# Performance work log

Measured on AMD Instinct MI355X. Metric: run time of the kernel, lower is better.

## Reference

```python
import jax, jax.numpy as jnp
import numpy as np

B, T, D, H = 512, 256, 64, 128


def _uniform(key, shape, stdv):
    return jax.random.uniform(key, shape, jnp.float32, -stdv, stdv)


def setup_inputs() -> dict:
    key = jax.random.key(0)
    ks = jax.random.split(key, 20)
    x_t = jax.random.normal(ks[0], (B, T, D), jnp.float32)
    masks = (jax.random.uniform(ks[1], (B, T, D)) < 0.8).astype(jnp.float32)
    deltas = jax.random.uniform(ks[2], (B, T, D), jnp.float32)
    sH = 1.0 / np.sqrt(H)
    sD = 1.0 / np.sqrt(D)
    return {
        "x_t": x_t, "masks": masks, "deltas": deltas,
        # TemporalDecay h: [H, D]
        "Wdh": _uniform(ks[3], (H, D), sH), "bdh": _uniform(ks[4], (H,), sH),
        # TemporalDecay x (diag): [D, D]
        "Wdx": _uniform(ks[5], (D, D), sD), "bdx": _uniform(ks[6], (D,), sD),
        # hist_reg Linear(H -> D)
        "Whr": _uniform(ks[7], (D, H), sH), "bhr": _uniform(ks[8], (D,), sH),
        "Wfr": _uniform(ks[9], (D, D), sD), "bfr": _uniform(ks[10], (D,), sD),
        # weight_combine Linear(2D -> D)
        "Wwc": _uniform(ks[11], (D, 2 * D), 1.0 / np.sqrt(2 * D)),
        "bwc": _uniform(ks[12], (D,), 1.0 / np.sqrt(2 * D)),
        # LSTMCell(2D -> H)
        "W_ih": _uniform(ks[13], (4 * H, 2 * D), sH), "W_hh": _uniform(ks[14], (4 * H, H), sH),
        "b_ih": _uniform(ks[15], (4 * H,), sH), "b_hh": _uniform(ks[16], (4 * H,), sH),
    }


def reference(x_t, masks, deltas, Wdh, bdh, Wdx, bdx, Whr, bhr, Wfr, bfr, Wwc, bwc, W_ih, W_hh, b_ih, b_hh):
    Bv, Tv, Dv = x_t.shape
    Hv = Wdh.shape[0]
    eye = jnp.eye(Dv, dtype=x_t.dtype)
    Wdx_m = Wdx * eye              # diagonal temporal decay
    Wfr_m = Wfr * (1.0 - eye)

    def step(carry, xs):
        h, c, loss = carry
        x, m, d = xs
        gamma_h = jnp.exp(-jax.nn.relu(d @ Wdh.T + bdh))   # [B,H]
        gamma_x = jnp.exp(-jax.nn.relu(d @ Wdx_m.T + bdx))  # [B,D]
        h = h * gamma_h
        x_h = h @ Whr.T + bhr
        msum = jnp.sum(m) + 1e-5
        loss = loss + jnp.sum(jnp.abs(x - x_h) * m) / msum
        x_c = m * x + (1.0 - m) * x_h
        z_h = x_c @ Wfr_m.T + bfr
        loss = loss + jnp.sum(jnp.abs(x - z_h) * m) / msum
        alpha = jnp.concatenate([gamma_x, m], axis=1) @ Wwc.T + bwc
        c_h = alpha * z_h + (1.0 - alpha) * x_h
        loss = loss + jnp.sum(jnp.abs(x - c_h) * m) / msum
        c_c = m * x + (1.0 - m) * c_h
        inp = jnp.concatenate([c_c, m], axis=1)            # [B,2D]
        gates = inp @ W_ih.T + b_ih + h @ W_hh.T + b_hh    # [B,4H]
        i, f, g, o = jnp.split(gates, 4, axis=1)
        c = jax.nn.sigmoid(f) * c + jax.nn.sigmoid(i) * jnp.tanh(g)
        h = jax.nn.sigmoid(o) * jnp.tanh(c)
        return (h, c, loss), c_c

    h0 = jnp.zeros((Bv, Hv), x_t.dtype)
    c0 = jnp.zeros((Bv, Hv), x_t.dtype)
    xs = (jnp.swapaxes(x_t, 0, 1), jnp.swapaxes(masks, 0, 1), jnp.swapaxes(deltas, 0, 1))
    (h, c, loss), imps = jax.lax.scan(step, (h0, c0, jnp.float32(0.0)), xs)
    imputations = jnp.swapaxes(imps, 0, 1)                 # [B,T,D]
    return loss / Tv, imputations
```

## Files before the change

### kernel.cpp

```cpp
#include <hip/hip_runtime.h>
#include <hip/hip_bf16.h>

typedef __bf16 bf16x8 __attribute__((ext_vector_type(8)));
typedef float f32x4 __attribute__((ext_vector_type(4)));

#define NB 512
#define NT 256
#define ND 64
#define NH 128
#define PART_IDX 256
#define FLAG_IDX 320

__device__ __forceinline__ float bf2f(__hip_bfloat16 v){ return __bfloat162float(v); }
__device__ __forceinline__ __hip_bfloat16 f2bf(float v){ return __float2bfloat16(v); }

__device__ __forceinline__ float ldF(const float* p){ return *p; }
__device__ __forceinline__ float ldF(const __hip_bfloat16* p){ return __bfloat162float(*p); }
__device__ __forceinline__ void  stF(float* p, float v){ *p = v; }
__device__ __forceinline__ void  stF(__hip_bfloat16* p, float v){ *p = __float2bfloat16(v); }

__device__ __forceinline__ bf16x8 ldfrag(const __hip_bfloat16* p){
    return *reinterpret_cast<const bf16x8*>(p);
}
__device__ __forceinline__ bf16x8 ldfrag(const float* p){
    f32x4 a = *reinterpret_cast<const f32x4*>(p);
    f32x4 b = *reinterpret_cast<const f32x4*>(p + 4);
    bf16x8 r;
    #pragma unroll
    for (int i = 0; i < 4; ++i){
        __hip_bfloat16 ha = __float2bfloat16(a[i]);
        __hip_bfloat16 hb = __float2bfloat16(b[i]);
        r[i]   = *reinterpret_cast<__bf16*>(&ha);
        r[4+i] = *reinterpret_cast<__bf16*>(&hb);
    }
    return r;
}
__device__ __forceinline__ bf16x8 ldbf8(const __hip_bfloat16* p){
    return *reinterpret_cast<const bf16x8*>(p);
}

template<typename T> __device__ __forceinline__ float wantFlag(){ return sizeof(T)==4 ? 1.f : 0.f; }

__device__ __forceinline__ f32x4 mfma16(bf16x8 a, bf16x8 b, f32x4 c){
    return __builtin_amdgcn_mfma_f32_16x16x32_bf16(a, b, c, 0, 0, 0);
}
__device__ __forceinline__ float fsig(float x){ return 1.f/(1.f+__expf(-x)); }
__device__ __forceinline__ float ftanh(float x){ return 1.f - 2.f/(__expf(2.f*x)+1.f); }

__global__ void detect_kernel(const void* __restrict__ x, float* __restrict__ WS){
    if (threadIdx.x == 0 && blockIdx.x == 0){
        const unsigned short* u = (const unsigned short*)x;
        int weird = 0;
        for (int i = 0; i < 256; ++i){
            unsigned e = (u[i] >> 7) & 0xFF;
            if (e == 0xFF || e >= 0x8A || (e != 0 && e <= 0x5A)) ++weird;
        }
        WS[FLAG_IDX] = (weird >= 16) ? 1.f : 0.f;
    }
}

template<typename T>
__global__ __launch_bounds__(256) void msum_kernel(const T* __restrict__ M,
                                                   float* __restrict__ WS){
    if (WS[FLAG_IDX] != wantFlag<T>()) return;
    int t = blockIdx.x;
    int tid = threadIdx.x;
    int col = tid & 63;
    int bg  = tid >> 6;
    float s = 0.f;
    for (int b = bg; b < NB; b += 4)
        s += ldF(&M[((size_t)b*NT + t)*ND + col]);
    #pragma unroll
    for (int off = 32; off > 0; off >>= 1) s += __shfl_down(s, off);
    __shared__ float r4[4];
    if ((tid & 63) == 0) r4[bg] = s;
    __syncthreads();
    if (tid == 0) WS[t] = 1.f / (r4[0] + r4[1] + r4[2] + r4[3] + 1e-5f);
}

template<typename T>
__device__ __forceinline__ f32x4 gates_tile(const T* __restrict__ wih_row,
                                            const T* __restrict__ whh_row,
                                            int lg, const bf16x8 af[8]){
    f32x4 acc = {0.f,0.f,0.f,0.f};
    acc = mfma16(af[0], ldfrag(wih_row + 0  + lg*8), acc);
    acc = mfma16(af[1], ldfrag(wih_row + 32 + lg*8), acc);
    acc = mfma16(af[2], ldfrag(wih_row + 64 + lg*8), acc);
    acc = mfma16(af[3], ldfrag(wih_row + 96 + lg*8), acc);
    acc = mfma16(af[4], ldfrag(whh_row + 0  + lg*8), acc);
    acc = mfma16(af[5], ldfrag(whh_row + 32 + lg*8), acc);
    acc = mfma16(af[6], ldfrag(whh_row + 64 + lg*8), acc);
    acc = mfma16(af[7], ldfrag(whh_row + 96 + lg*8), acc);
    return acc;
}

template<typename T>
__global__ __launch_bounds__(512, 2) void brits_main(
    const T* __restrict__ X,  const T* __restrict__ M,
    const T* __restrict__ DL,
    const T* __restrict__ Wdh, const T* __restrict__ bdh,
    const T* __restrict__ Wdx, const T* __restrict__ bdx,
    const T* __restrict__ Whr, const T* __restrict__ bhr,
    const T* __restrict__ Wfr, const T* __restrict__ bfr,
    const T* __restrict__ Wwc, const T* __restrict__ bwc,
    const T* __restrict__ Wih, const T* __restrict__ Whh,
    const T* __restrict__ bih, const T* __restrict__ bhh,
    T* __restrict__ OUT, float* __restrict__ WS)
{
    if (WS[FLAG_IDX] != wantFlag<T>()) return;

    __shared__ __align__(16) __hip_bfloat16 sAg[16][264];
    __shared__ __align__(16) __hip_bfloat16 sAal[16][136];
    __shared__ __align__(16) __hip_bfloat16 sXc[16][72];
    __shared__ __align__(16) T sX[16][72];
    __shared__ float sXh[16][68];
    __shared__ float sZh[16][68];
    __shared__ float sAl[16][68];
    __shared__ float sWdg[64];
    __shared__ float sBdx[64];
    __shared__ float sRed[8];

    const int tid = threadIdx.x;
    const int w  = tid >> 6;
    const int l  = tid & 63;
    const int lr = l & 15;
    const int lg = l >> 4;
    const int b0 = blockIdx.x * 16;

    if (tid < 64){ sWdg[tid] = ldF(&Wdx[tid*ND + tid]); sBdx[tid] = ldF(&bdx[tid]); }

    const int hcol = 16*w + lr;
    const float bdh_r = ldF(&bdh[hcol]);
    const float gb_i = ldF(&bih[hcol])      + ldF(&bhh[hcol]);
    const float gb_f = ldF(&bih[NH+hcol])   + ldF(&bhh[NH+hcol]);
    const float gb_g = ldF(&bih[2*NH+hcol]) + ldF(&bhh[2*NH+hcol]);
    const float gb_o = ldF(&bih[3*NH+hcol]) + ldF(&bhh[3*NH+hcol]);

    bf16x8 pB0 = ldfrag(Wdh + (size_t)hcol*ND + lg*8);
    bf16x8 pB1 = ldfrag(Wdh + (size_t)hcol*ND + 32 + lg*8);
    bf16x8 qB0 = {}, qB1 = {}, qB2 = {}, qB3 = {}, rB0 = {}, rB1 = {};
    float b1_r = 0.f, b2_r = 0.f, b3_r = 0.f;
    int dcol;
    if (w < 4){
        dcol = 16*w + lr;
        b1_r = ldF(&bhr[dcol]);  b2_r = ldF(&bfr[dcol]);
        qB0 = ldfrag(Whr + (size_t)dcol*NH + lg*8);
        qB1 = ldfrag(Whr + (size_t)dcol*NH + 32 + lg*8);
        qB2 = ldfrag(Whr + (size_t)dcol*NH + 64 + lg*8);
        qB3 = ldfrag(Whr + (size_t)dcol*NH + 96 + lg*8);
        rB0 = ldfrag(Wfr + (size_t)dcol*ND + lg*8);
        rB1 = ldfrag(Wfr + (size_t)dcol*ND + 32 + lg*8);
        int kb0 = lg*8;      if (dcol >= kb0 && dcol < kb0+8) rB0[dcol-kb0] = (__bf16)0.f;
        int kb1 = 32 + lg*8; if (dcol >= kb1 && dcol < kb1+8) rB1[dcol-kb1] = (__bf16)0.f;
    } else {
        dcol = 16*(w-4) + lr;
        b3_r = ldF(&bwc[dcol]);
        qB0 = ldfrag(Wwc + (size_t)dcol*2*ND + lg*8);
        qB1 = ldfrag(Wwc + (size_t)dcol*2*ND + 32 + lg*8);
        qB2 = ldfrag(Wwc + (size_t)dcol*2*ND + 64 + lg*8);
        qB3 = ldfrag(Wwc + (size_t)dcol*2*ND + 96 + lg*8);
    }

    float hreg[4] = {0.f,0.f,0.f,0.f};
    float creg[4] = {0.f,0.f,0.f,0.f};
    float lacc = 0.f;

    const int r0 = tid >> 5;
    const int c0 = (tid & 31) * 2;

    __syncthreads();

    #pragma unroll 1
    for (int t = 0; t < NT; ++t){
        const float inv_ms = WS[t];
        {
            const T* drow = DL + ((size_t)(b0+lr)*NT + t)*ND;
            f32x4 acc = {0.f,0.f,0.f,0.f};
            acc = mfma16(ldfrag(drow + lg*8), pB0, acc);
            acc = mfma16(ldfrag(drow + 32 + lg*8), pB1, acc);
            #pragma unroll
            for (int r = 0; r < 4; ++r){
                float gm = __expf(-fmaxf(acc[r] + bdh_r, 0.f));
                hreg[r] *= gm;
                sAg[lg*4+r][128 + hcol] = f2bf(hreg[r]);
            }
            #pragma unroll
            for (int e = 0; e < 2; ++e){
                int row = r0, col = c0 + e;
                size_t g = ((size_t)(b0+row)*NT + t)*ND + col;
                float dv = ldF(&DL[g]);
                float gx = __expf(-fmaxf(dv*sWdg[col] + sBdx[col], 0.f));
                sAal[row][col] = f2bf(gx);
                float mv = ldF(&M[g]);
                sAal[row][64+col] = f2bf(mv);
                sAg[row][64+col]  = f2bf(mv);
                sX[row][col]      = X[g];
            }
        }
        __syncthreads();
        if (w < 4){
            f32x4 acc = {0.f,0.f,0.f,0.f};
            acc = mfma16(ldbf8(&sAg[lr][128 + 0  + lg*8]), qB0, acc);
            acc = mfma16(ldbf8(&sAg[lr][128 + 32 + lg*8]), qB1, acc);
            acc = mfma16(ldbf8(&sAg[lr][128 + 64 + lg*8]), qB2, acc);
            acc = mfma16(ldbf8(&sAg[lr][128 + 96 + lg*8]), qB3, acc);
            #pragma unroll
            for (int r = 0; r < 4; ++r){
                int row = lg*4 + r;
                float xh = acc[r] + b1_r;
                sXh[row][dcol] = xh;
                float mv = bf2f(sAg[row][64+dcol]);
                float xv = ldF(&sX[row][dcol]);
                float xc = mv*xv + (1.f-mv)*xh;
                sXc[row][dcol] = f2bf(xc);
                lacc += fabsf(xv - xh) * mv * inv_ms;
            }
        } else {
            f32x4 acc = {0.f,0.f,0.f,0.f};
            acc = mfma16(ldbf8(&sAal[lr][0  + lg*8]), qB0, acc);
            acc = mfma16(ldbf8(&sAal[lr][32 + lg*8]), qB1, acc);
            acc = mfma16(ldbf8(&sAal[lr][64 + lg*8]), qB2, acc);
            acc = mfma16(ldbf8(&sAal[lr][96 + lg*8]), qB3, acc);
            #pragma unroll
            for (int r = 0; r < 4; ++r) sAl[lg*4+r][dcol] = acc[r] + b3_r;
        }
        __syncthreads();
        if (w < 4){
            f32x4 acc = {0.f,0.f,0.f,0.f};
            acc = mfma16(ldbf8(&sXc[lr][0  + lg*8]), rB0, acc);
            acc = mfma16(ldbf8(&sXc[lr][32 + lg*8]), rB1, acc);
            #pragma unroll
            for (int r = 0; r < 4; ++r) sZh[lg*4+r][dcol] = acc[r] + b2_r;
        }
        __syncthreads();
        {
            #pragma unroll
            for (int e = 0; e < 2; ++e){
                int row = r0, col = c0 + e;
                size_t g = ((size_t)(b0+row)*NT + t)*ND + col;
                float xv = ldF(&sX[row][col]);
                float mv = bf2f(sAg[row][64+col]);
                float zh = sZh[row][col];
                float xh = sXh[row][col];
                float al = sAl[row][col];
                float ch = al*zh + (1.f-al)*xh;
                lacc += (fabsf(xv - zh) + fabsf(xv - ch)) * mv * inv_ms;
                float cc = mv*xv + (1.f-mv)*ch;
                stF(&OUT[1 + g], cc);
                sAg[row][col] = f2bf(cc);
            }
        }
        __syncthreads();
        {
            bf16x8 af[8];
            #pragma unroll
            for (int kk = 0; kk < 8; ++kk) af[kk] = ldbf8(&sAg[lr][kk*32 + lg*8]);
            f32x4 a_i = gates_tile(Wih + (size_t)(hcol)*128,        Whh + (size_t)(hcol)*128,        lg, af);
            f32x4 a_f = gates_tile(Wih + (size_t)(NH   + hcol)*128, Whh + (size_t)(NH   + hcol)*128, lg, af);
            f32x4 a_g = gates_tile(Wih + (size_t)(2*NH + hcol)*128, Whh + (size_t)(2*NH + hcol)*128, lg, af);
            f32x4 a_o = gates_tile(Wih + (size_t)(3*NH + hcol)*128, Whh + (size_t)(3*NH + hcol)*128, lg, af);
            #pragma unroll
            for (int r = 0; r < 4; ++r){
                float iv = fsig(a_i[r] + gb_i);
                float fv = fsig(a_f[r] + gb_f);
                float gv = ftanh(a_g[r] + gb_g);
                float ov = fsig(a_o[r] + gb_o);
                creg[r] = fv*creg[r] + iv*gv;
                hreg[r] = ov*ftanh(creg[r]);
            }
        }
        __syncthreads();
    }

    #pragma unroll
    for (int off = 32; off > 0; off >>= 1) lacc += __shfl_down(lacc, off);
    if (l == 0) sRed[w] = lacc;
    __syncthreads();
    if (tid == 0){
        float s = 0.f;
        #pragma unroll
        for (int i = 0; i < 8; ++i) s += sRed[i];
        WS[PART_IDX + blockIdx.x] = s;
    }
}

template<typename T>
__global__ void fin_kernel(const float* __restrict__ WS, T* __restrict__ OUT){
    if (WS[FLAG_IDX] != wantFlag<T>()) return;
    if (threadIdx.x == 0 && blockIdx.x == 0){
        float s = 0.f;
        for (int i = 0; i < 32; ++i) s += WS[PART_IDX + i];
        stF(&OUT[0], s / (float)NT);
    }
}

template<typename T>
static void launch_all(void* const* d_in, void* d_out, float* WS, hipStream_t stream){
    const T* X   = (const T*)d_in[0];
    const T* M   = (const T*)d_in[1];
    const T* DL  = (const T*)d_in[2];
    const T* Wdh = (const T*)d_in[3];
    const T* bdh = (const T*)d_in[4];
    const T* Wdx = (const T*)d_in[5];
    const T* bdx = (const T*)d_in[6];
    const T* Whr = (const T*)d_in[7];
    const T* bhr = (const T*)d_in[8];
    const T* Wfr = (const T*)d_in[9];
    const T* bfr = (const T*)d_in[10];
    const T* Wwc = (const T*)d_in[11];
    const T* bwc = (const T*)d_in[12];
    const T* Wih = (const T*)d_in[13];
    const T* Whh = (const T*)d_in[14];
    const T* bih = (const T*)d_in[15];
    const T* bhh = (const T*)d_in[16];
    T* OUT = (T*)d_out;
    msum_kernel<T><<<dim3(NT), dim3(256), 0, stream>>>(M, WS);
    brits_main<T><<<dim3(32), dim3(512), 0, stream>>>(X, M, DL, Wdh, bdh, Wdx, bdx,
                                                      Whr, bhr, Wfr, bfr, Wwc, bwc,
                                                      Wih, Whh, bih, bhh, OUT, WS);
    fin_kernel<T><<<dim3(1), dim3(64), 0, stream>>>(WS, OUT);
}

extern "C" void kernel_launch(void* const* d_in, const int* in_sizes, int n_in,
                              void* d_out, int out_size, void* d_ws, size_t ws_size,
                              hipStream_t stream) {
    float* WS = (float*)d_ws;
    detect_kernel<<<dim3(1), dim3(64), 0, stream>>>(d_in[0], WS);
    launch_all<__hip_bfloat16>(d_in, d_out, WS, stream);
    launch_all<float>(d_in, d_out, WS, stream);
}
```

Before: 900.4 us.

## Keep LSTM weights in registers, prefetch next step inputs, split gate GEMM

The LSTM input and recurrent weight fragments now load once into registers instead of being re-read from global memory every timestep. The next timestep's deltas, masks and x are prefetched during the current step, and the decay factors for the next step are computed early. Most of the gate GEMM (the h and mask parts) is issued before the imputation chain, so only the c_c part stays on the critical path, and one barrier per step is removed. The cost is a large rise in register use (32 extra bf16x8 fragments), which may hurt occupancy at 512 threads or cause spills.

```diff
diff --git a/kernel.cpp b/kernel.cpp
--- a/kernel.cpp
+++ b/kernel.cpp
@@ -38,6 +38,33 @@
 __device__ __forceinline__ bf16x8 ldbf8(const __hip_bfloat16* p){
     return *reinterpret_cast<const bf16x8*>(p);
 }
+
+template<typename T> struct PF;
+template<> struct PF<float>{
+    f32x4 a, b;
+    __device__ __forceinline__ void load(const float* p){
+        a = *reinterpret_cast<const f32x4*>(p);
+        b = *reinterpret_cast<const f32x4*>(p + 4);
+    }
+    __device__ __forceinline__ bf16x8 get() const {
+        bf16x8 r;
+        #pragma unroll
+        for (int i = 0; i < 4; ++i){
+            __hip_bfloat16 ha = __float2bfloat16(a[i]);
+            __hip_bfloat16 hb = __float2bfloat16(b[i]);
+            r[i]   = *reinterpret_cast<const __bf16*>(&ha);
+            r[4+i] = *reinterpret_cast<const __bf16*>(&hb);
+        }
+        return r;
+    }
+};
+template<> struct PF<__hip_bfloat16>{
+    bf16x8 a;
+    __device__ __forceinline__ void load(const __hip_bfloat16* p){
+        a = *reinterpret_cast<const bf16x8*>(p);
+    }
+    __device__ __forceinline__ bf16x8 get() const { return a; }
+};
 
 template<typename T> __device__ __forceinline__ float wantFlag(){ return sizeof(T)==4 ? 1.f : 0.f; }
 
@@ -76,22 +103,6 @@
     if ((tid & 63) == 0) r4[bg] = s;
     __syncthreads();
     if (tid == 0) WS[t] = 1.f / (r4[0] + r4[1] + r4[2] + r4[3] + 1e-5f);
-}
-
-template<typename T>
-__device__ __forceinline__ f32x4 gates_tile(const T* __restrict__ wih_row,
-                                            const T* __restrict__ whh_row,
-                                            int lg, const bf16x8 af[8]){
-    f32x4 acc = {0.f,0.f,0.f,0.f};
-    acc = mfma16(af[0], ldfrag(wih_row + 0  + lg*8), acc);
-    acc = mfma16(af[1], ldfrag(wih_row + 32 + lg*8), acc);
-    acc = mfma16(af[2], ldfrag(wih_row + 64 + lg*8), acc);
-    acc = mfma16(af[3], ldfrag(wih_row + 96 + lg*8), acc);
-    acc = mfma16(af[4], ldfrag(whh_row + 0  + lg*8), acc);
-    acc = mfma16(af[5], ldfrag(whh_row + 32 + lg*8), acc);
-    acc = mfma16(af[6], ldfrag(whh_row + 64 + lg*8), acc);
-    acc = mfma16(af[7], ldfrag(whh_row + 96 + lg*8), acc);
-    return acc;
 }
 
 template<typename T>
@@ -109,15 +120,13 @@
 {
     if (WS[FLAG_IDX] != wantFlag<T>()) return;
 
-    __shared__ __align__(16) __hip_bfloat16 sAg[16][264];
-    __shared__ __align__(16) __hip_bfloat16 sAal[16][136];
-    __shared__ __align__(16) __hip_bfloat16 sXc[16][72];
+    __shared__ __align__(16) __hip_bfloat16 sH [16][136];
+    __shared__ __align__(16) __hip_bfloat16 sGM[16][136];
+    __shared__ __align__(16) __hip_bfloat16 sCX[16][72];
     __shared__ __align__(16) T sX[16][72];
     __shared__ float sXh[16][68];
     __shared__ float sZh[16][68];
     __shared__ float sAl[16][68];
-    __shared__ float sWdg[64];
-    __shared__ float sBdx[64];
     __shared__ float sRed[8];
 
     const int tid = threadIdx.x;
@@ -126,8 +135,6 @@
     const int lr = l & 15;
     const int lg = l >> 4;
     const int b0 = blockIdx.x * 16;
-
-    if (tid < 64){ sWdg[tid] = ldF(&Wdx[tid*ND + tid]); sBdx[tid] = ldF(&bdx[tid]); }
 
     const int hcol = 16*w + lr;
     const float bdh_r = ldF(&bdh[hcol]);
@@ -160,113 +167,162 @@
         qB2 = ldfrag(Wwc + (size_t)dcol*2*ND + 64 + lg*8);
         qB3 = ldfrag(Wwc + (size_t)dcol*2*ND + 96 + lg*8);
     }
+    bf16x8 Wg[4][8];
+    #pragma unroll
+    for (int g = 0; g < 4; ++g){
+        const T* wr = Wih + (size_t)(g*NH + hcol)*128;
+        const T* hr = Whh + (size_t)(g*NH + hcol)*128;
+        #pragma unroll
+        for (int kk = 0; kk < 4; ++kk) Wg[g][kk]   = ldfrag(wr + kk*32 + lg*8);
+        #pragma unroll
+        for (int kk = 0; kk < 4; ++kk) Wg[g][4+kk] = ldfrag(hr + kk*32 + lg*8);
+    }
+
+    const int r0 = tid >> 5;
+    const int c0 = (tid & 31) * 2;
+    const float wdg0 = ldF(&Wdx[(size_t)c0*ND + c0]);
+    const float wdg1 = ldF(&Wdx[(size_t)(c0+1)*ND + (c0+1)]);
+    const float bdx0 = ldF(&bdx[c0]);
+    const float bdx1 = ldF(&bdx[c0+1]);
 
     float hreg[4] = {0.f,0.f,0.f,0.f};
     float creg[4] = {0.f,0.f,0.f,0.f};
+    float gh_next[4];
     float lacc = 0.f;
 
-    const int r0 = tid >> 5;
-    const int c0 = (tid & 31) * 2;
-
+    #pragma unroll
+    for (int r = 0; r < 4; ++r) sH[lg*4+r][hcol] = f2bf(0.f);
+    {
+        size_t g0 = ((size_t)(b0+r0)*NT + 0)*ND + c0;
+        float d0 = ldF(&DL[g0]), d1 = ldF(&DL[g0+1]);
+        sGM[r0][c0]    = f2bf(__expf(-fmaxf(d0*wdg0 + bdx0, 0.f)));
+        sGM[r0][c0+1]  = f2bf(__expf(-fmaxf(d1*wdg1 + bdx1, 0.f)));
+        sGM[r0][64+c0]   = f2bf(ldF(&M[g0]));
+        sGM[r0][64+c0+1] = f2bf(ldF(&M[g0+1]));
+        sX[r0][c0]   = X[g0];
+        sX[r0][c0+1] = X[g0+1];
+    }
     __syncthreads();
 
     #pragma unroll 1
     for (int t = 0; t < NT; ++t){
         const float inv_ms = WS[t];
-        {
-            const T* drow = DL + ((size_t)(b0+lr)*NT + t)*ND;
-            f32x4 acc = {0.f,0.f,0.f,0.f};
-            acc = mfma16(ldfrag(drow + lg*8), pB0, acc);
-            acc = mfma16(ldfrag(drow + 32 + lg*8), pB1, acc);
-            #pragma unroll
-            for (int r = 0; r < 4; ++r){
-                float gm = __expf(-fmaxf(acc[r] + bdh_r, 0.f));
-                hreg[r] *= gm;
-                sAg[lg*4+r][128 + hcol] = f2bf(hreg[r]);
-            }
-            #pragma unroll
-            for (int e = 0; e < 2; ++e){
-                int row = r0, col = c0 + e;
-                size_t g = ((size_t)(b0+row)*NT + t)*ND + col;
-                float dv = ldF(&DL[g]);
-                float gx = __expf(-fmaxf(dv*sWdg[col] + sBdx[col], 0.f));
-                sAal[row][col] = f2bf(gx);
-                float mv = ldF(&M[g]);
-                sAal[row][64+col] = f2bf(mv);
-                sAg[row][64+col]  = f2bf(mv);
-                sX[row][col]      = X[g];
-            }
-        }
-        __syncthreads();
+        const int tn = (t+1 < NT) ? t+1 : t;
+        bf16x8 ah0 = ldbf8(&sH[lr][0   + lg*8]);
+        bf16x8 ah1 = ldbf8(&sH[lr][32  + lg*8]);
+        bf16x8 ah2 = ldbf8(&sH[lr][64  + lg*8]);
+        bf16x8 ah3 = ldbf8(&sH[lr][96  + lg*8]);
+        bf16x8 am0 = ldbf8(&sGM[lr][64 + lg*8]);
+        bf16x8 am1 = ldbf8(&sGM[lr][96 + lg*8]);
+
+        PF<T> pfA0, pfA1;
+        const T* drow = DL + ((size_t)(b0+lr)*NT + tn)*ND;
+        pfA0.load(drow + lg*8);
+        pfA1.load(drow + 32 + lg*8);
+        size_t gE = ((size_t)(b0+r0)*NT + tn)*ND + c0;
+        float pd0 = ldF(&DL[gE]), pd1 = ldF(&DL[gE+1]);
+        float pm0 = ldF(&M[gE]),  pm1 = ldF(&M[gE+1]);
+        T     px0 = X[gE],        px1 = X[gE+1];
+
+        f32x4 gacc[4];
+        #pragma unroll
+        for (int g = 0; g < 4; ++g){
+            f32x4 a = {0.f,0.f,0.f,0.f};
+            a = mfma16(ah0, Wg[g][4], a);
+            a = mfma16(ah1, Wg[g][5], a);
+            a = mfma16(ah2, Wg[g][6], a);
+            a = mfma16(ah3, Wg[g][7], a);
+            a = mfma16(am0, Wg[g][2], a);
+            a = mfma16(am1, Wg[g][3], a);
+            gacc[g] = a;
+        }
         if (w < 4){
             f32x4 acc = {0.f,0.f,0.f,0.f};
-            acc = mfma16(ldbf8(&sAg[lr][128 + 0  + lg*8]), qB0, acc);
-            acc = mfma16(ldbf8(&sAg[lr][128 + 32 + lg*8]), qB1, acc);
-            acc = mfma16(ldbf8(&sAg[lr][128 + 64 + lg*8]), qB2, acc);
-            acc = mfma16(ldbf8(&sAg[lr][128 + 96 + lg*8]), qB3, acc);
+            acc = mfma16(ah0, qB0, acc);
+            acc = mfma16(ah1, qB1, acc);
+            acc = mfma16(ah2, qB2, acc);
+            acc = mfma16(ah3, qB3, acc);
             #pragma unroll
             for (int r = 0; r < 4; ++r){
                 int row = lg*4 + r;
                 float xh = acc[r] + b1_r;
                 sXh[row][dcol] = xh;
-                float mv = bf2f(sAg[row][64+dcol]);
+                float mv = bf2f(sGM[row][64+dcol]);
                 float xv = ldF(&sX[row][dcol]);
                 float xc = mv*xv + (1.f-mv)*xh;
-                sXc[row][dcol] = f2bf(xc);
+                sCX[row][dcol] = f2bf(xc);
                 lacc += fabsf(xv - xh) * mv * inv_ms;
             }
         } else {
             f32x4 acc = {0.f,0.f,0.f,0.f};
-            acc = mfma16(ldbf8(&sAal[lr][0  + lg*8]), qB0, acc);
-            acc = mfma16(ldbf8(&sAal[lr][32 + lg*8]), qB1, acc);
-            acc = mfma16(ldbf8(&sAal[lr][64 + lg*8]), qB2, acc);
-            acc = mfma16(ldbf8(&sAal[lr][96 + lg*8]), qB3, acc);
+            acc = mfma16(ldbf8(&sGM[lr][0  + lg*8]), qB0, acc);
+            acc = mfma16(ldbf8(&sGM[lr][32 + lg*8]), qB1, acc);
+            acc = mfma16(am0, qB2, acc);
+            acc = mfma16(am1, qB3, acc);
             #pragma unroll
             for (int r = 0; r < 4; ++r) sAl[lg*4+r][dcol] = acc[r] + b3_r;
         }
         __syncthreads();
         if (w < 4){
             f32x4 acc = {0.f,0.f,0.f,0.f};
-            acc = mfma16(ldbf8(&sXc[lr][0  + lg*8]), rB0, acc);
-            acc = mfma16(ldbf8(&sXc[lr][32 + lg*8]), rB1, acc);
+            acc = mfma16(ldbf8(&sCX[lr][0  + lg*8]), rB0, acc);
+            acc = mfma16(ldbf8(&sCX[lr][32 + lg*8]), rB1, acc);
             #pragma unroll
             for (int r = 0; r < 4; ++r) sZh[lg*4+r][dcol] = acc[r] + b2_r;
         }
+        {
+            f32x4 acc = {0.f,0.f,0.f,0.f};
+            acc = mfma16(pfA0.get(), pB0, acc);
+            acc = mfma16(pfA1.get(), pB1, acc);
+            #pragma unroll
+            for (int r = 0; r < 4; ++r)
+                gh_next[r] = __expf(-fmaxf(acc[r] + bdh_r, 0.f));
+        }
+        float gx0 = __expf(-fmaxf(pd0*wdg0 + bdx0, 0.f));
+        float gx1 = __expf(-fmaxf(pd1*wdg1 + bdx1, 0.f));
         __syncthreads();
         {
+            size_t g = ((size_t)(b0+r0)*NT + t)*ND + c0;
             #pragma unroll
             for (int e = 0; e < 2; ++e){
-                int row = r0, col = c0 + e;
-                size_t g = ((size_t)(b0+row)*NT + t)*ND + col;
-                float xv = ldF(&sX[row][col]);
-                float mv = bf2f(sAg[row][64+col]);
-                float zh = sZh[row][col];
-                float xh = sXh[row][col];
-                float al = sAl[row][col];
+                int col = c0 + e;
+                float xv = ldF(&sX[r0][col]);
+                float mv = bf2f(sGM[r0][64+col]);
+                float zh = sZh[r0][col];
+                float xh = sXh[r0][col];
+                float al = sAl[r0][col];
                 float ch = al*zh + (1.f-al)*xh;
                 lacc += (fabsf(xv - zh) + fabsf(xv - ch)) * mv * inv_ms;
                 float cc = mv*xv + (1.f-mv)*ch;
-                stF(&OUT[1 + g], cc);
-                sAg[row][col] = f2bf(cc);
+                stF(&OUT[1 + g + e], cc);
+                sCX[r0][col] = f2bf(cc);
             }
+            sGM[r0][c0]      = f2bf(gx0);
+            sGM[r0][c0+1]    = f2bf(gx1);
+            sGM[r0][64+c0]   = f2bf(pm0);
+            sGM[r0][64+c0+1] = f2bf(pm1);
+            sX[r0][c0]   = px0;
+            sX[r0][c0+1] = px1;
         }
         __syncthreads();
         {
-            bf16x8 af[8];
-            #pragma unroll
-            for (int kk = 0; kk < 8; ++kk) af[kk] = ldbf8(&sAg[lr][kk*32 + lg*8]);
-            f32x4 a_i = gates_tile(Wih + (size_t)(hcol)*128,        Whh + (size_t)(hcol)*128,        lg, af);
-            f32x4 a_f = gates_tile(Wih + (size_t)(NH   + hcol)*128, Whh + (size_t)(NH   + hcol)*128, lg, af);
-            f32x4 a_g = gates_tile(Wih + (size_t)(2*NH + hcol)*128, Whh + (size_t)(2*NH + hcol)*128, lg, af);
-            f32x4 a_o = gates_tile(Wih + (size_t)(3*NH + hcol)*128, Whh + (size_t)(3*NH + hcol)*128, lg, af);
+            bf16x8 ac0 = ldbf8(&sCX[lr][0  + lg*8]);
+            bf16x8 ac1 = ldbf8(&sCX[lr][32 + lg*8]);
+            #pragma unroll
+            for (int g = 0; g < 4; ++g){
+                gacc[g] = mfma16(ac0, Wg[g][0], gacc[g]);
+                gacc[g] = mfma16(ac1, Wg[g][1], gacc[g]);
+            }
             #pragma unroll
             for (int r = 0; r < 4; ++r){
-                float iv = fsig(a_i[r] + gb_i);
-                float fv = fsig(a_f[r] + gb_f);
-                float gv = ftanh(a_g[r] + gb_g);
-                float ov = fsig(a_o[r] + gb_o);
+                float iv = fsig(gacc[0][r] + gb_i);
+                float fv = fsig(gacc[1][r] + gb_f);
+                float gv = ftanh(gacc[2][r] + gb_g);
+                float ov = fsig(gacc[3][r] + gb_o);
                 creg[r] = fv*creg[r] + iv*gv;
-                hreg[r] = ov*ftanh(creg[r]);
+                float hn = ov*ftanh(creg[r]);
+                hreg[r] = hn * gh_next[r];
+                sH[lg*4+r][hcol] = f2bf(hreg[r]);
             }
         }
         __syncthreads();
```

After: 1.035 ms. +15.0%, slower.

## Pre-pack LSTM weights into MFMA fragment order and keep W_hh in LDS

Applied to the files above, without the earlier changes.

Adds a pack kernel that writes W_ih and W_hh into bf16 MFMA-fragment order in the workspace. The main kernel copies the packed W_hh (128 KB) into dynamic LDS and reads W_ih fragments with coalesced loads, so the per-step float-to-bf16 conversion and strided global weight reads go away. It also vectorizes the per-step x/m/delta loads into pairs and moves the diagonal decay weights into registers. The large dynamic LDS allocation limits occupancy to one block per CU, and the packing adds an extra launch.

```diff
diff --git a/kernel.cpp b/kernel.cpp
--- a/kernel.cpp
+++ b/kernel.cpp
@@ -10,6 +10,8 @@
 #define NH 128
 #define PART_IDX 256
 #define FLAG_IDX 320
+#define PACK_OFF 8192
+#define NFRAG 8192
 
 __device__ __forceinline__ float bf2f(__hip_bfloat16 v){ return __bfloat162float(v); }
 __device__ __forceinline__ __hip_bfloat16 f2bf(float v){ return __float2bfloat16(v); }
@@ -18,6 +20,16 @@
 __device__ __forceinline__ float ldF(const __hip_bfloat16* p){ return __bfloat162float(*p); }
 __device__ __forceinline__ void  stF(float* p, float v){ *p = v; }
 __device__ __forceinline__ void  stF(__hip_bfloat16* p, float v){ *p = __float2bfloat16(v); }
+
+__device__ __forceinline__ void ld2(const float* p, float& a, float& b){
+    float2 v = *reinterpret_cast<const float2*>(p); a = v.x; b = v.y;
+}
+__device__ __forceinline__ void ld2(const __hip_bfloat16* p, float& a, float& b){
+    unsigned u = *reinterpret_cast<const unsigned*>(p);
+    unsigned short s0 = (unsigned short)(u & 0xffffu), s1 = (unsigned short)(u >> 16);
+    a = __bfloat162float(*reinterpret_cast<__hip_bfloat16*>(&s0));
+    b = __bfloat162float(*reinterpret_cast<__hip_bfloat16*>(&s1));
+}
 
 __device__ __forceinline__ bf16x8 ldfrag(const __hip_bfloat16* p){
     return *reinterpret_cast<const bf16x8*>(p);
@@ -57,6 +69,24 @@
         }
         WS[FLAG_IDX] = (weird >= 16) ? 1.f : 0.f;
     }
+}
+
+template<typename T>
+__global__ __launch_bounds__(256) void pack_kernel(const T* __restrict__ Wih,
+                                                   const T* __restrict__ Whh,
+                                                   float* __restrict__ WS){
+    if (WS[FLAG_IDX] != wantFlag<T>()) return;
+    int f = blockIdx.x * 256 + threadIdx.x;
+    int l  = f & 63;
+    int w  = (f >> 6) & 7;
+    int kk = (f >> 9) & 3;
+    int g  = (f >> 11) & 3;
+    int lr = l & 15, lg = l >> 4;
+    size_t row = (size_t)(g*NH + 16*w + lr);
+    int col = kk*32 + lg*8;
+    bf16x8* PW = (bf16x8*)((char*)WS + PACK_OFF);
+    PW[f]         = ldfrag(Wih + row*128 + col);
+    PW[NFRAG + f] = ldfrag(Whh + row*128 + col);
 }
 
 template<typename T>
@@ -79,22 +109,6 @@
 }
 
 template<typename T>
-__device__ __forceinline__ f32x4 gates_tile(const T* __restrict__ wih_row,
-                                            const T* __restrict__ whh_row,
-                                            int lg, const bf16x8 af[8]){
-    f32x4 acc = {0.f,0.f,0.f,0.f};
-    acc = mfma16(af[0], ldfrag(wih_row + 0  + lg*8), acc);
-    acc = mfma16(af[1], ldfrag(wih_row + 32 + lg*8), acc);
-    acc = mfma16(af[2], ldfrag(wih_row + 64 + lg*8), acc);
-    acc = mfma16(af[3], ldfrag(wih_row + 96 + lg*8), acc);
-    acc = mfma16(af[4], ldfrag(whh_row + 0  + lg*8), acc);
-    acc = mfma16(af[5], ldfrag(whh_row + 32 + lg*8), acc);
-    acc = mfma16(af[6], ldfrag(whh_row + 64 + lg*8), acc);
-    acc = mfma16(af[7], ldfrag(whh_row + 96 + lg*8), acc);
-    return acc;
-}
-
-template<typename T>
 __global__ __launch_bounds__(512, 2) void brits_main(
     const T* __restrict__ X,  const T* __restrict__ M,
     const T* __restrict__ DL,
@@ -112,13 +126,13 @@
     __shared__ __align__(16) __hip_bfloat16 sAg[16][264];
     __shared__ __align__(16) __hip_bfloat16 sAal[16][136];
     __shared__ __align__(16) __hip_bfloat16 sXc[16][72];
-    __shared__ __align__(16) T sX[16][72];
+    __shared__ float sX [16][68];
     __shared__ float sXh[16][68];
     __shared__ float sZh[16][68];
     __shared__ float sAl[16][68];
-    __shared__ float sWdg[64];
-    __shared__ float sBdx[64];
     __shared__ float sRed[8];
+    extern __shared__ __align__(16) char dynLDS[];
+    bf16x8* sWhh = (bf16x8*)dynLDS;
 
     const int tid = threadIdx.x;
     const int w  = tid >> 6;
@@ -127,7 +141,11 @@
     const int lg = l >> 4;
     const int b0 = blockIdx.x * 16;
 
-    if (tid < 64){ sWdg[tid] = ldF(&Wdx[tid*ND + tid]); sBdx[tid] = ldF(&bdx[tid]); }
+    const bf16x8* PW = (const bf16x8*)((const char*)WS + PACK_OFF);
+    const bf16x8* PH = PW + NFRAG;
+
+    #pragma unroll
+    for (int i = 0; i < 16; ++i) sWhh[tid + i*512] = PH[tid + i*512];
 
     const int hcol = 16*w + lr;
     const float bdh_r = ldF(&bdh[hcol]);
@@ -161,12 +179,16 @@
         qB3 = ldfrag(Wwc + (size_t)dcol*2*ND + 96 + lg*8);
     }
 
+    const int r0 = tid >> 5;
+    const int c0 = (tid & 31) * 2;
+    const float wdg0 = ldF(&Wdx[(size_t)c0*ND + c0]);
+    const float wdg1 = ldF(&Wdx[(size_t)(c0+1)*ND + (c0+1)]);
+    const float bdx0 = ldF(&bdx[c0]);
+    const float bdx1 = ldF(&bdx[c0+1]);
+
     float hreg[4] = {0.f,0.f,0.f,0.f};
     float creg[4] = {0.f,0.f,0.f,0.f};
     float lacc = 0.f;
-
-    const int r0 = tid >> 5;
-    const int c0 = (tid & 31) * 2;
 
     __syncthreads();
 
@@ -184,18 +206,19 @@
                 hreg[r] *= gm;
                 sAg[lg*4+r][128 + hcol] = f2bf(hreg[r]);
             }
-            #pragma unroll
-            for (int e = 0; e < 2; ++e){
-                int row = r0, col = c0 + e;
-                size_t g = ((size_t)(b0+row)*NT + t)*ND + col;
-                float dv = ldF(&DL[g]);
-                float gx = __expf(-fmaxf(dv*sWdg[col] + sBdx[col], 0.f));
-                sAal[row][col] = f2bf(gx);
-                float mv = ldF(&M[g]);
-                sAal[row][64+col] = f2bf(mv);
-                sAg[row][64+col]  = f2bf(mv);
-                sX[row][col]      = X[g];
-            }
+            size_t gE = ((size_t)(b0+r0)*NT + t)*ND + c0;
+            float d0, d1, m0, m1, x0, x1;
+            ld2(DL + gE, d0, d1); ld2(M + gE, m0, m1); ld2(X + gE, x0, x1);
+            float gx0 = __expf(-fmaxf(d0*wdg0 + bdx0, 0.f));
+            float gx1 = __expf(-fmaxf(d1*wdg1 + bdx1, 0.f));
+            sAal[r0][c0]      = f2bf(gx0);
+            sAal[r0][c0+1]    = f2bf(gx1);
+            sAal[r0][64+c0]   = f2bf(m0);
+            sAal[r0][64+c0+1] = f2bf(m1);
+            sAg[r0][64+c0]    = f2bf(m0);
+            sAg[r0][64+c0+1]  = f2bf(m1);
+            sX[r0][c0]   = x0;
+            sX[r0][c0+1] = x1;
         }
         __syncthreads();
         if (w < 4){
@@ -210,7 +233,7 @@
                 float xh = acc[r] + b1_r;
                 sXh[row][dcol] = xh;
                 float mv = bf2f(sAg[row][64+dcol]);
-                float xv = ldF(&sX[row][dcol]);
+                float xv = sX[row][dcol];
                 float xc = mv*xv + (1.f-mv)*xh;
                 sXc[row][dcol] = f2bf(xc);
                 lacc += fabsf(xv - xh) * mv * inv_ms;
@@ -234,20 +257,20 @@
         }
         __syncthreads();
         {
+            size_t g = ((size_t)(b0+r0)*NT + t)*ND + c0;
             #pragma unroll
             for (int e = 0; e < 2; ++e){
-                int row = r0, col = c0 + e;
-                size_t g = ((size_t)(b0+row)*NT + t)*ND + col;
-                float xv = ldF(&sX[row][col]);
-                float mv = bf2f(sAg[row][64+col]);
-                float zh = sZh[row][col];
-                float xh = sXh[row][col];
-                float al = sAl[row][col];
+                int col = c0 + e;
+                float xv = sX[r0][col];
+                float mv = bf2f(sAg[r0][64+col]);
+                float zh = sZh[r0][col];
+                float xh = sXh[r0][col];
+                float al = sAl[r0][col];
                 float ch = al*zh + (1.f-al)*xh;
                 lacc += (fabsf(xv - zh) + fabsf(xv - ch)) * mv * inv_ms;
                 float cc = mv*xv + (1.f-mv)*ch;
-                stF(&OUT[1 + g], cc);
-                sAg[row][col] = f2bf(cc);
+                stF(&OUT[1 + g + e], cc);
+                sAg[r0][col] = f2bf(cc);
             }
         }
         __syncthreads();
@@ -255,16 +278,31 @@
             bf16x8 af[8];
             #pragma unroll
             for (int kk = 0; kk < 8; ++kk) af[kk] = ldbf8(&sAg[lr][kk*32 + lg*8]);
-            f32x4 a_i = gates_tile(Wih + (size_t)(hcol)*128,        Whh + (size_t)(hcol)*128,        lg, af);
-            f32x4 a_f = gates_tile(Wih + (size_t)(NH   + hcol)*128, Whh + (size_t)(NH   + hcol)*128, lg, af);
-            f32x4 a_g = gates_tile(Wih + (size_t)(2*NH + hcol)*128, Whh + (size_t)(2*NH + hcol)*128, lg, af);
-            f32x4 a_o = gates_tile(Wih + (size_t)(3*NH + hcol)*128, Whh + (size_t)(3*NH + hcol)*128, lg, af);
+            const int wb = w*64 + l;
+            f32x4 gacc[4];
+            #pragma unroll
+            for (int g = 0; g < 4; ++g){
+                const bf16x8* pw = PW + g*2048 + wb;
+                bf16x8 w0 = pw[0], w1 = pw[512], w2 = pw[1024], w3 = pw[1536];
+                const bf16x8* ph = sWhh + g*2048 + wb;
+                bf16x8 h0 = ph[0], h1 = ph[512], h2 = ph[1024], h3 = ph[1536];
+                f32x4 a = {0.f,0.f,0.f,0.f};
+                a = mfma16(af[0], w0, a);
+                a = mfma16(af[1], w1, a);
+                a = mfma16(af[2], w2, a);
+                a = mfma16(af[3], w3, a);
+                a = mfma16(af[4], h0, a);
+                a = mfma16(af[5], h1, a);
+                a = mfma16(af[6], h2, a);
+                a = mfma16(af[7], h3, a);
+                gacc[g] = a;
+            }
             #pragma unroll
             for (int r = 0; r < 4; ++r){
-                float iv = fsig(a_i[r] + gb_i);
-                float fv = fsig(a_f[r] + gb_f);
-                float gv = ftanh(a_g[r] + gb_g);
-                float ov = fsig(a_o[r] + gb_o);
+                float iv = fsig(gacc[0][r] + gb_i);
+                float fv = fsig(gacc[1][r] + gb_f);
+                float gv = ftanh(gacc[2][r] + gb_g);
+                float ov = fsig(gacc[3][r] + gb_o);
                 creg[r] = fv*creg[r] + iv*gv;
                 hreg[r] = ov*ftanh(creg[r]);
             }
@@ -314,10 +352,20 @@
     const T* bih = (const T*)d_in[15];
     const T* bhh = (const T*)d_in[16];
     T* OUT = (T*)d_out;
+
+    static bool attr_done_f32 = false, attr_done_bf16 = false;
+    bool& attr_done = (sizeof(T) == 4) ? attr_done_f32 : attr_done_bf16;
+    if (!attr_done){
+        (void)hipFuncSetAttribute((const void*)brits_main<T>,
+                                  hipFuncAttributeMaxDynamicSharedMemorySize, 131072);
+        attr_done = true;
+    }
+
+    pack_kernel<T><<<dim3(32), dim3(256), 0, stream>>>(Wih, Whh, WS);
     msum_kernel<T><<<dim3(NT), dim3(256), 0, stream>>>(M, WS);
-    brits_main<T><<<dim3(32), dim3(512), 0, stream>>>(X, M, DL, Wdh, bdh, Wdx, bdx,
-                                                      Whr, bhr, Wfr, bfr, Wwc, bwc,
-                                                      Wih, Whh, bih, bhh, OUT, WS);
+    brits_main<T><<<dim3(32), dim3(512), 131072, stream>>>(X, M, DL, Wdh, bdh, Wdx, bdx,
+                                                           Whr, bhr, Wfr, bfr, Wwc, bwc,
+                                                           Wih, Whh, bih, bhh, OUT, WS);
     fin_kernel<T><<<dim3(1), dim3(64), 0, stream>>>(WS, OUT);
 }
 
```

After: 1.199 ms. 33.1% more time.
